# Kernel optimization log

Hardware: AMD Instinct MI355X
Metric: run time of the kernel (lower is better)

The kernel has to match this reference:

```python
import jax, jax.numpy as jnp
import numpy as np

N, E, G = 200000, 1200000, 2048
NODE_DIM, H = 5, 64
NEG_SLOPE = 0.2


def setup_inputs() -> dict:
    key = jax.random.key(0)
    ks = jax.random.split(key, 20)
    def glorot(k, shape):
        fan = sum(shape) if len(shape) > 1 else shape[0] + 1
        return jax.random.normal(k, shape, jnp.float32) * jnp.sqrt(2.0 / fan)
    inp = {
        'x': jax.random.normal(ks[0], (N, NODE_DIM), jnp.float32),
        'edge_index': jax.random.randint(ks[1], (2, E), 0, N, jnp.int64),
        'batch': jnp.sort(jax.random.randint(ks[2], (N,), 0, G, jnp.int64)),
        'embed_W': glorot(ks[3], (NODE_DIM, H)), 'embed_b': jnp.zeros((H,), jnp.float32),
        'g1_W': glorot(ks[4], (H, H)), 'g1_asrc': glorot(ks[5], (H,)), 'g1_adst': glorot(ks[6], (H,)), 'g1_b': jnp.zeros((H,), jnp.float32),
        'g2_W': glorot(ks[7], (H, H)), 'g2_asrc': glorot(ks[8], (H,)), 'g2_adst': glorot(ks[9], (H,)), 'g2_b': jnp.zeros((H,), jnp.float32),
        'fc1_W': glorot(ks[10], (2 * H, 64)), 'fc1_b': jnp.zeros((64,), jnp.float32),
        'fc2_W': glorot(ks[11], (64, 32)), 'fc2_b': jnp.zeros((32,), jnp.float32),
        'fc3_W': glorot(ks[12], (32, 1)), 'fc3_b': jnp.zeros((1,), jnp.float32),
    }
    return inp


def gat_conv(x, src, dst, W, a_src, a_dst, b):
    # x: [N, H] -> h: [N, H]; edges (with self-loops) src->dst
    h = x @ W
    alpha_s = h @ a_src  # [N]
    alpha_d = h @ a_dst  # [N]
    e = jax.nn.leaky_relu(alpha_s[src] + alpha_d[dst], NEG_SLOPE)  # [E']
    m = jax.ops.segment_max(e, dst, num_segments=N)
    w = jnp.exp(e - m[dst])
    denom = jax.ops.segment_sum(w, dst, num_segments=N)
    alpha = w / (denom[dst] + 1e-16)
    out = jax.ops.segment_sum(h[src] * alpha[:, None], dst, num_segments=N)
    return out + b


def reference(x, edge_index, batch, embed_W, embed_b,
              g1_W, g1_asrc, g1_adst, g1_b,
              g2_W, g2_asrc, g2_adst, g2_b,
              fc1_W, fc1_b, fc2_W, fc2_b, fc3_W, fc3_b):
    # add self loops once (PyG GATConv default add_self_loops=True)
    loops = jnp.arange(N, dtype=edge_index.dtype)
    src = jnp.concatenate([edge_index[0], loops])
    dst = jnp.concatenate([edge_index[1], loops])

    h = x @ embed_W + embed_b
    h = gat_conv(h, src, dst, g1_W, g1_asrc, g1_adst, g1_b)
    h = jax.nn.relu(h)
    h = gat_conv(h, src, dst, g2_W, g2_asrc, g2_adst, g2_b)

    # global mean / max pooling per graph
    cnt = jax.ops.segment_sum(jnp.ones((N,), h.dtype), batch, num_segments=G)
    mean = jax.ops.segment_sum(h, batch, num_segments=G) / jnp.maximum(cnt, 1.0)[:, None]
    mx = jax.ops.segment_max(h, batch, num_segments=G)
    mx = jnp.where(cnt[:, None] > 0, mx, 0.0)
    g = jnp.concatenate([mean, mx], axis=1)  # [G, 2H]

    g = jax.nn.relu(g @ fc1_W + fc1_b)
    g = jax.nn.relu(g @ fc2_W + fc2_b)
    return g @ fc3_W + fc3_b  # [G, 1]
```

## Files before the change

### kernel.cpp

```cpp
#include <hip/hip_runtime.h>
#include <hip/hip_bf16.h>
#include <hip/hip_fp16.h>

#define HD 64
#define NODE_DIM 5
#define NEG_SLOPE 0.2f
#define GT 64
#define BSH 9
#define BNODES 512
#define NBMAX 512
#define BCAP 4096
#define EPB 8
#define LDH 72

typedef _Float16 f16x8 __attribute__((ext_vector_type(8)));
typedef float f32x4 __attribute__((ext_vector_type(4)));


__global__ void zero_k(int* __restrict__ p, int total) {
    int i = blockIdx.x * blockDim.x + threadIdx.x;
    if (i < total) p[i] = 0;
}

union FusedSM {
    struct {
        _Float16 hs[GT * LDH];
        _Float16 Wt[HD * LDH];
        float xe[GT * NODE_DIM];
        float we[NODE_DIM * HD + HD];
    } g;
    struct {
        int lcnt[NBMAX];
        int lbase[NBMAX];
        int lexc[NBMAX];
        int cur[NBMAX];
        int sorted[256 * EPB];
    } p;
};

__global__ __launch_bounds__(256) void fused_embed_part_k(
    const float* __restrict__ xin, const float* __restrict__ embW,
    const float* __restrict__ embB, const float* __restrict__ W,
    const float* __restrict__ asrc, const float* __restrict__ adst,
    __half* __restrict__ hout, float* __restrict__ alpha_s,
    float* __restrict__ alpha_d, int N,
    const int* __restrict__ ei, int* __restrict__ bcnt,
    int* __restrict__ bpack, int E, int PB, int TOT) {
    __shared__ FusedSM sm;
    const int t = threadIdx.x;
    const int bid = blockIdx.x;
    const int p_before = (int)(((long long)bid * PB) / TOT);
    const int p_after  = (int)(((long long)(bid + 1) * PB) / TOT);
    const bool is_part = p_after > p_before;

    if (is_part) {
        const int pbid = p_before;
        int dst[EPB], src[EPB];
        int jb = pbid * (256 * EPB) + t;
#pragma unroll
        for (int u = 0; u < EPB; u++) {
            int j = jb + u * 256;
            if (j < E) {
                dst[u] = __builtin_nontemporal_load(&ei[E + j]);
                src[u] = __builtin_nontemporal_load(&ei[j]);
            } else dst[u] = -1;
        }
        sm.p.lcnt[t] = 0; sm.p.lcnt[t + 256] = 0;
        __syncthreads();
#pragma unroll
        for (int u = 0; u < EPB; u++)
            if (dst[u] >= 0) atomicAdd(&sm.p.lcnt[dst[u] >> BSH], 1);
        __syncthreads();
        sm.p.lexc[t] = sm.p.lcnt[t];
        sm.p.lexc[t + 256] = sm.p.lcnt[t + 256];
        __syncthreads();
        int c0 = sm.p.lexc[t], c1 = sm.p.lexc[t + 256];
#pragma unroll
        for (int o = 1; o < NBMAX; o <<= 1) {
            int a0 = (t >= o) ? sm.p.lexc[t - o] : 0;
            int a1 = (t + 256 >= o) ? sm.p.lexc[t + 256 - o] : 0;
            __syncthreads();
            sm.p.lexc[t] += a0;
            sm.p.lexc[t + 256] += a1;
            __syncthreads();
        }
        int e0 = sm.p.lexc[t] - c0, e1 = sm.p.lexc[t + 256] - c1;
        __syncthreads();
        sm.p.lexc[t] = e0; sm.p.lexc[t + 256] = e1;
        sm.p.cur[t] = e0;  sm.p.cur[t + 256] = e1;
        {
            int c = sm.p.lcnt[t];
            sm.p.lbase[t] = c ? t * BCAP + atomicAdd(&bcnt[t], c) : 0;
            c = sm.p.lcnt[t + 256];
            sm.p.lbase[t + 256] = c ? (t + 256) * BCAP + atomicAdd(&bcnt[t + 256], c) : 0;
        }
        __syncthreads();
#pragma unroll
        for (int u = 0; u < EPB; u++) {
            if (dst[u] >= 0) {
                int b = dst[u] >> BSH;
                int pp = atomicAdd(&sm.p.cur[b], 1);
                sm.p.sorted[pp] = (src[u] << BSH) | (dst[u] & (BNODES - 1));
            }
        }
        __syncthreads();
        const int tot = sm.p.lexc[NBMAX - 1] + sm.p.lcnt[NBMAX - 1];
        for (int j = t; j < tot; j += 256) {
            int lo = 0, hi = NBMAX - 1;
            while (lo < hi) {
                int mid = (lo + hi + 1) >> 1;
                if (sm.p.lexc[mid] <= j) lo = mid; else hi = mid - 1;
            }
            bpack[sm.p.lbase[lo] + (j - sm.p.lexc[lo])] = sm.p.sorted[j];
        }
        return;
    }

    const int gidx = bid - p_before;
    const int n0 = gidx * GT;
    if (n0 >= N) return;
    const int rem = N - n0;

#pragma unroll
    for (int j = 0; j < 16; j++) {
        int idx = t + 256 * j;
        int k = idx >> 6, n = idx & 63;
        sm.g.Wt[n * LDH + k] = (_Float16)W[idx];
    }
    for (int j = t; j < GT * NODE_DIM; j += 256)
        sm.g.xe[j] = (j < rem * NODE_DIM) ? xin[(size_t)n0 * NODE_DIM + j] : 0.0f;
    for (int j = t; j < NODE_DIM * HD + HD; j += 256)
        sm.g.we[j] = (j < NODE_DIM * HD) ? embW[j] : embB[j - NODE_DIM * HD];
    __syncthreads();
    {
        int r = t >> 2, d0 = (t & 3) * 16;
#pragma unroll
        for (int jj = 0; jj < 16; jj++) {
            int d = d0 + jj;
            float acc = sm.g.we[NODE_DIM * HD + d];
#pragma unroll
            for (int k = 0; k < NODE_DIM; k++)
                acc = fmaf(sm.g.xe[r * NODE_DIM + k], sm.g.we[k * HD + d], acc);
            sm.g.hs[r * LDH + d] = (r < rem) ? (_Float16)acc : (_Float16)0.0f;
        }
    }
    __syncthreads();

    const int lane = t & 63;
    const int w = t >> 6;
    const int r16 = lane & 15;
    const int g = lane >> 4;

    const _Float16* hrow = sm.g.hs + (w * 16 + r16) * LDH + g * 8;
    f16x8 b0 = *(const f16x8*)(hrow);
    f16x8 b1 = *(const f16x8*)(hrow + 32);

    f32x4 acc[4];
#pragma unroll
    for (int mt = 0; mt < 4; mt++) acc[mt] = (f32x4){0.f, 0.f, 0.f, 0.f};
#pragma unroll
    for (int mt = 0; mt < 4; mt++) {
        const _Float16* arow = sm.g.Wt + (mt * 16 + r16) * LDH + g * 8;
        f16x8 a0 = *(const f16x8*)(arow);
        f16x8 a1 = *(const f16x8*)(arow + 32);
        acc[mt] = __builtin_amdgcn_mfma_f32_16x16x32_f16(a0, b0, acc[mt], 0, 0, 0);
        acc[mt] = __builtin_amdgcn_mfma_f32_16x16x32_f16(a1, b1, acc[mt], 0, 0, 0);
    }

    const int node = n0 + w * 16 + r16;
    float ps = 0.0f, pd = 0.0f;
    if (node < N) {
#pragma unroll
        for (int mt = 0; mt < 4; mt++) {
            float4 av = ((const float4*)asrc)[mt * 4 + g];
            float4 bv = ((const float4*)adst)[mt * 4 + g];
            ps += acc[mt][0] * av.x + acc[mt][1] * av.y +
                  acc[mt][2] * av.z + acc[mt][3] * av.w;
            pd += acc[mt][0] * bv.x + acc[mt][1] * bv.y +
                  acc[mt][2] * bv.z + acc[mt][3] * bv.w;
            short4 s;
            s.x = __half_as_short(__float2half_rn(acc[mt][0]));
            s.y = __half_as_short(__float2half_rn(acc[mt][1]));
            s.z = __half_as_short(__float2half_rn(acc[mt][2]));
            s.w = __half_as_short(__float2half_rn(acc[mt][3]));
            ((short4*)hout)[(size_t)node * 16 + mt * 4 + g] = s;
        }
    }
    ps += __shfl_xor(ps, 16);
    ps += __shfl_xor(ps, 32);
    pd += __shfl_xor(pd, 16);
    pd += __shfl_xor(pd, 32);
    if (g == 0 && node < N) {
        alpha_s[node] = ps;
        alpha_d[node] = pd;
    }
}

__global__ __launch_bounds__(256) void gemm_alpha_k(
    const __half* __restrict__ hin, const float* __restrict__ W,
    const float* __restrict__ asrc, const float* __restrict__ adst,
    __half* __restrict__ hout, float* __restrict__ alpha_s,
    float* __restrict__ alpha_d, int N) {
    __shared__ _Float16 hs[GT * LDH];
    __shared__ _Float16 Wt[HD * LDH];
    const int t = threadIdx.x;
    const int n0 = blockIdx.x * GT;
    if (n0 >= N) return;
    const int rem = N - n0;

#pragma unroll
    for (int j = 0; j < 16; j++) {
        int idx = t + 256 * j;
        int k = idx >> 6, n = idx & 63;
        Wt[n * LDH + k] = (_Float16)W[idx];
    }
    {
        const short4* g4 = (const short4*)(hin + (size_t)n0 * HD);
#pragma unroll
        for (int j = 0; j < 4; j++) {
            int idx = t + 256 * j;
            int row = idx >> 4, c4 = idx & 15;
            short4 v = {0, 0, 0, 0};
            if (row < rem) v = g4[idx];
            *(short4*)(hs + row * LDH + c4 * 4) = v;
        }
    }
    __syncthreads();

    const int lane = t & 63;
    const int w = t >> 6;
    const int r16 = lane & 15;
    const int g = lane >> 4;

    const _Float16* hrow = hs + (w * 16 + r16) * LDH + g * 8;
    f16x8 b0 = *(const f16x8*)(hrow);
    f16x8 b1 = *(const f16x8*)(hrow + 32);

    f32x4 acc[4];
#pragma unroll
    for (int mt = 0; mt < 4; mt++) acc[mt] = (f32x4){0.f, 0.f, 0.f, 0.f};
#pragma unroll
    for (int mt = 0; mt < 4; mt++) {
        const _Float16* arow = Wt + (mt * 16 + r16) * LDH + g * 8;
        f16x8 a0 = *(const f16x8*)(arow);
        f16x8 a1 = *(const f16x8*)(arow + 32);
        acc[mt] = __builtin_amdgcn_mfma_f32_16x16x32_f16(a0, b0, acc[mt], 0, 0, 0);
        acc[mt] = __builtin_amdgcn_mfma_f32_16x16x32_f16(a1, b1, acc[mt], 0, 0, 0);
    }

    const int node = n0 + w * 16 + r16;
    float ps = 0.0f, pd = 0.0f;
    if (node < N) {
#pragma unroll
        for (int mt = 0; mt < 4; mt++) {
            float4 av = ((const float4*)asrc)[mt * 4 + g];
            float4 bv = ((const float4*)adst)[mt * 4 + g];
            ps += acc[mt][0] * av.x + acc[mt][1] * av.y +
                  acc[mt][2] * av.z + acc[mt][3] * av.w;
            pd += acc[mt][0] * bv.x + acc[mt][1] * bv.y +
                  acc[mt][2] * bv.z + acc[mt][3] * bv.w;
            short4 s;
            s.x = __half_as_short(__float2half_rn(acc[mt][0]));
            s.y = __half_as_short(__float2half_rn(acc[mt][1]));
            s.z = __half_as_short(__float2half_rn(acc[mt][2]));
            s.w = __half_as_short(__float2half_rn(acc[mt][3]));
            ((short4*)hout)[(size_t)node * 16 + mt * 4 + g] = s;
        }
    }
    ps += __shfl_xor(ps, 16);
    ps += __shfl_xor(ps, 32);
    pd += __shfl_xor(pd, 16);
    pd += __shfl_xor(pd, 32);
    if (g == 0 && node < N) {
        alpha_s[node] = ps;
        alpha_d[node] = pd;
    }
}

__global__ __launch_bounds__(256) void bucket_csr_k(
    const int* __restrict__ bpack, const int* __restrict__ bcnt,
    int* __restrict__ off, int* __restrict__ csr_src, int N, int NB) {
    __shared__ int s[BNODES];
    __shared__ int lcur[BNODES];
    __shared__ int sred[256];
    const int t = threadIdx.x;
    const int b = blockIdx.x;
    const int nbase = b << BSH;
    const int cnt = bcnt[b];
    const int w0 = b * BCAP;

    int part = 0;
    for (int j = t; j < b; j += 256) part += bcnt[j];
    sred[t] = part;
    s[t] = 0; s[t + 256] = 0;
    __syncthreads();
#pragma unroll
    for (int o = 128; o; o >>= 1) {
        if (t < o) sred[t] += sred[t + o];
        __syncthreads();
    }
    const int e0 = sred[0];

    for (int j = t; j < cnt; j += 256)
        atomicAdd(&s[bpack[w0 + j] & (BNODES - 1)], 1);
    __syncthreads();
    int d0 = s[t], d1 = s[t + 256];
#pragma unroll
    for (int o = 1; o < BNODES; o <<= 1) {
        int a0 = (t >= o) ? s[t - o] : 0;
        int a1 = (t + 256 >= o) ? s[t + 256 - o] : 0;
        __syncthreads();
        s[t] += a0;
        s[t + 256] += a1;
        __syncthreads();
    }
    int ex0 = s[t] - d0, ex1 = s[t + 256] - d1;
    lcur[t] = ex0; lcur[t + 256] = ex1;
    int n0 = nbase + t, n1 = nbase + t + 256;
    if (n0 < N) off[n0] = e0 + ex0;
    if (n1 < N) off[n1] = e0 + ex1;
    if (t == 0 && b == NB - 1) off[N] = e0 + cnt;
    __syncthreads();
    for (int j = t; j < cnt; j += 256) {
        int v = bpack[w0 + j];
        int pos = atomicAdd(&lcur[v & (BNODES - 1)], 1);
        csr_src[e0 + pos] = v >> BSH;
    }
}

template <bool BR>
__global__ __launch_bounds__(256) void gather_k(
    const int* __restrict__ off, const int* __restrict__ csr_src,
    const float* __restrict__ as, const float* __restrict__ ad,
    const __half* __restrict__ h, const float* __restrict__ bias,
    __half* __restrict__ out, int N) {
    int tid = blockIdx.x * blockDim.x + threadIdx.x;
    int wv = tid >> 6;
    int lane = threadIdx.x & 63;
    int grp = lane >> 4;
    int l16 = lane & 15;
    int n = wv * 4 + grp;
    if (n >= N) return;
    int s0 = off[n], s1 = off[n + 1];
    float adv = ad[n];
    const short4* h4 = (const short4*)h;

    float e = as[n] + adv;
    e = (e >= 0.0f) ? e : NEG_SLOPE * e;
    float wsl = __expf(e);
    float l0 = wsl, l1 = 0.0f;
    short4 hvs = h4[(unsigned)(n * 16 + l16)];
    float4 acc0, acc1 = {0, 0, 0, 0};
    acc0.x = wsl * __half2float(__short_as_half(hvs.x));
    acc0.y = wsl * __half2float(__short_as_half(hvs.y));
    acc0.z = wsl * __half2float(__short_as_half(hvs.z));
    acc0.w = wsl * __half2float(__short_as_half(hvs.w));

    const int last = s1 - 1;
    for (int i = s0; i < s1; i += 8) {
        int src[8];
        short4 hv[8];
        float wt[8];
#pragma unroll
        for (int u = 0; u < 8; u++) {
            int idx = i + u;
            src[u] = csr_src[idx < s1 ? idx : last];
        }
#pragma unroll
        for (int u = 0; u < 8; u++)
            hv[u] = h4[(unsigned)(src[u] * 16 + l16)];
#pragma unroll
        for (int u = 0; u < 8; u++) {
            float e0 = as[src[u]] + adv;
            e0 = (e0 >= 0.0f) ? e0 : NEG_SLOPE * e0;
            float w0 = __expf(e0);
            wt[u] = (i + u < s1) ? w0 : 0.0f;
        }
#pragma unroll
        for (int u = 0; u < 8; u += 2) {
            l0 += wt[u];
            l1 += wt[u + 1];
            acc0.x = fmaf(wt[u], __half2float(__short_as_half(hv[u].x)), acc0.x);
            acc0.y = fmaf(wt[u], __half2float(__short_as_half(hv[u].y)), acc0.y);
            acc0.z = fmaf(wt[u], __half2float(__short_as_half(hv[u].z)), acc0.z);
            acc0.w = fmaf(wt[u], __half2float(__short_as_half(hv[u].w)), acc0.w);
            acc1.x = fmaf(wt[u + 1], __half2float(__short_as_half(hv[u + 1].x)), acc1.x);
            acc1.y = fmaf(wt[u + 1], __half2float(__short_as_half(hv[u + 1].y)), acc1.y);
            acc1.z = fmaf(wt[u + 1], __half2float(__short_as_half(hv[u + 1].z)), acc1.z);
            acc1.w = fmaf(wt[u + 1], __half2float(__short_as_half(hv[u + 1].w)), acc1.w);
        }
    }
    float inv = 1.0f / (l0 + l1 + 1e-16f);
    float4 r;
    r.x = (acc0.x + acc1.x) * inv;
    r.y = (acc0.y + acc1.y) * inv;
    r.z = (acc0.z + acc1.z) * inv;
    r.w = (acc0.w + acc1.w) * inv;
    if (BR) {
        float4 b = ((const float4*)bias)[l16];
        r.x = fmaxf(r.x + b.x, 0.0f);
        r.y = fmaxf(r.y + b.y, 0.0f);
        r.z = fmaxf(r.z + b.z, 0.0f);
        r.w = fmaxf(r.w + b.w, 0.0f);
    }
    short4 o;
    o.x = __half_as_short(__float2half_rn(r.x));
    o.y = __half_as_short(__float2half_rn(r.y));
    o.z = __half_as_short(__float2half_rn(r.z));
    o.w = __half_as_short(__float2half_rn(r.w));
    ((short4*)out)[(unsigned)(n * 16 + l16)] = o;
}

__global__ __launch_bounds__(256) void pool_mlp_k(
    const __half* __restrict__ hfin, const float* __restrict__ hb,
    const int* __restrict__ batch, int N,
    const float* __restrict__ fc1W, const float* __restrict__ fc1b,
    const float* __restrict__ fc2W, const float* __restrict__ fc2b,
    const float* __restrict__ fc3W, const float* __restrict__ fc3b,
    float* __restrict__ out) {
    __shared__ float psum[16][64];
    __shared__ float pmax[16][64];
    __shared__ float lds[192];
    int g = blockIdx.x;
    int t = threadIdx.x;
    int gg = t >> 4;
    int l16 = t & 15;
    int lo = 0, hi = N;
    while (lo < hi) { int mid = (lo + hi) >> 1; if (batch[mid] < g) lo = mid + 1; else hi = mid; }
    int start = lo;
    lo = start; hi = N;
    while (lo < hi) { int mid = (lo + hi) >> 1; if (batch[mid] < g + 1) lo = mid + 1; else hi = mid; }
    int end = lo;
    const short4* h4 = (const short4*)hfin;
    float4 sum = {0, 0, 0, 0};
    float4 mx = {-INFINITY, -INFINITY, -INFINITY, -INFINITY};
    for (int n = start + gg; n < end; n += 16) {
        short4 v = h4[(size_t)n * 16 + l16];
        float a = __half2float(__short_as_half(v.x));
        float b = __half2float(__short_as_half(v.y));
        float c = __half2float(__short_as_half(v.z));
        float d = __half2float(__short_as_half(v.w));
        sum.x += a; sum.y += b; sum.z += c; sum.w += d;
        mx.x = fmaxf(mx.x, a); mx.y = fmaxf(mx.y, b);
        mx.z = fmaxf(mx.z, c); mx.w = fmaxf(mx.w, d);
    }
    *(float4*)&psum[gg][l16 * 4] = sum;
    *(float4*)&pmax[gg][l16 * 4] = mx;
    __syncthreads();
    if (t < 64) {
        float s = 0.0f, m = -INFINITY;
#pragma unroll
        for (int k = 0; k < 16; k++) {
            s += psum[k][t];
            m = fmaxf(m, pmax[k][t]);
        }
        int cnt = end - start;
        float bias = hb[t];
        lds[t]      = (cnt > 0) ? s / (float)cnt + bias : 0.0f;
        lds[64 + t] = (cnt > 0) ? m + bias : 0.0f;
    }
    __syncthreads();
    if (t < 64) {
        int lane = t;
        float o1 = fc1b[lane];
        for (int k = 0; k < 128; k++) o1 += lds[k] * fc1W[k * 64 + lane];
        o1 = fmaxf(o1, 0.0f);
        __builtin_amdgcn_s_barrier();
        lds[128 + lane] = o1;
        float o2 = 0.0f;
        if (lane < 32) {
            o2 = fc2b[lane];
            for (int k = 0; k < 64; k++) o2 += lds[128 + k] * fc2W[k * 32 + lane];
            o2 = fmaxf(o2, 0.0f);
        }
        float part = (lane < 32) ? o2 * fc3W[lane] : 0.0f;
#pragma unroll
        for (int off = 32; off; off >>= 1) part += __shfl_xor(part, off);
        if (lane == 0) out[g] = part + fc3b[0];
    }
}

static inline size_t align256(size_t x) { return (x + 255) & ~(size_t)255; }

extern "C" void kernel_launch(void* const* d_in, const int* in_sizes, int n_in,
                              void* d_out, int out_size, void* d_ws, size_t ws_size,
                              hipStream_t stream) {
    const float* x      = (const float*)d_in[0];
    const int*   ei     = (const int*)d_in[1];
    const int*   batch  = (const int*)d_in[2];
    const float* embW   = (const float*)d_in[3];
    const float* embB   = (const float*)d_in[4];
    const float* g1W    = (const float*)d_in[5];
    const float* g1as   = (const float*)d_in[6];
    const float* g1ad   = (const float*)d_in[7];
    const float* g1b    = (const float*)d_in[8];
    const float* g2W    = (const float*)d_in[9];
    const float* g2as   = (const float*)d_in[10];
    const float* g2ad   = (const float*)d_in[11];
    const float* g2b    = (const float*)d_in[12];
    const float* fc1W   = (const float*)d_in[13];
    const float* fc1b   = (const float*)d_in[14];
    const float* fc2W   = (const float*)d_in[15];
    const float* fc2b   = (const float*)d_in[16];
    const float* fc3W   = (const float*)d_in[17];
    const float* fc3b   = (const float*)d_in[18];
    float* out = (float*)d_out;

    const int N  = in_sizes[0] / NODE_DIM;
    const int E  = in_sizes[1] / 2;
    const int G  = out_size;
    const int NH = N * HD;
    const int NB = (N + BNODES - 1) >> BSH;

    char* ws = (char*)d_ws;
    __half* bufA    = (__half*)ws; ws += align256((size_t)NH * 2);
    __half* bufB    = (__half*)ws; ws += align256((size_t)NH * 2);
    float*  as_buf  = (float*)ws;  ws += align256((size_t)N * 4);
    float*  ad_buf  = (float*)ws;  ws += align256((size_t)N * 4);
    int*    off     = (int*)ws;    ws += align256((size_t)(N + 1) * 4);
    int*    bcnt    = (int*)ws;    ws += align256((size_t)NBMAX * 4);
    int*    bpack   = (int*)ws;    ws += align256((size_t)NB * BCAP * 4);
    int*    csrsrc  = (int*)ws;    ws += align256((size_t)E * 4);

    const int B = 256;
    dim3 blk(B);
    const int GB = (N + GT - 1) / GT;
    const int PB = (E + B * EPB - 1) / (B * EPB);
    const int TOT = GB + PB;
    dim3 gr_gath(((N + 3) / 4 * 64 + B - 1) / B);

    zero_k<<<dim3(2), blk, 0, stream>>>(bcnt, NBMAX);
    fused_embed_part_k<<<dim3(TOT), blk, 0, stream>>>(
        x, embW, embB, g1W, g1as, g1ad, bufB, as_buf, ad_buf, N,
        ei, bcnt, bpack, E, PB, TOT);
    bucket_csr_k<<<dim3(NB), blk, 0, stream>>>(bpack, bcnt, off, csrsrc, N, NB);

    gather_k<true><<<gr_gath, blk, 0, stream>>>(off, csrsrc, as_buf, ad_buf,
                                                bufB, g1b, bufA, N);

    gemm_alpha_k<<<dim3(GB), blk, 0, stream>>>(bufA, g2W, g2as, g2ad,
                                               bufB, as_buf, ad_buf, N);
    gather_k<false><<<gr_gath, blk, 0, stream>>>(off, csrsrc, as_buf, ad_buf,
                                                 bufB, nullptr, bufA, N);

    pool_mlp_k<<<dim3(G), dim3(256), 0, stream>>>(bufA, g2b, batch, N,
                                                  fc1W, fc1b, fc2W, fc2b, fc3W, fc3b, out);
}
```

Baseline: 256.5 us.

## Fuse second GAT gather into per-graph pooling and MLP kernel

Drops the separate second-layer gather kernel and does the attention-weighted neighbor aggregation inside the per-graph pool kernel, which now runs 512 threads per graph. Each 16-lane group handles one node, rounds the result to half precision to match the old stored values, and feeds it straight into the sum/max pooling. This removes one launch and the write and re-read of the full N×64 half-precision intermediate. In exchange, parallelism is now bounded by 2048 graph blocks with uneven node counts, which may cost load balance compared with the old node-parallel gather.

```diff
diff --git a/kernel.cpp b/kernel.cpp
--- a/kernel.cpp
+++ b/kernel.cpp
@@ -411,46 +411,108 @@
     ((short4*)out)[(unsigned)(n * 16 + l16)] = o;
 }
 
-__global__ __launch_bounds__(256) void pool_mlp_k(
-    const __half* __restrict__ hfin, const float* __restrict__ hb,
+__global__ __launch_bounds__(512) void gather_pool_mlp_k(
+    const int* __restrict__ off, const int* __restrict__ csr_src,
+    const float* __restrict__ as, const float* __restrict__ ad,
+    const __half* __restrict__ h, const float* __restrict__ hb,
     const int* __restrict__ batch, int N,
     const float* __restrict__ fc1W, const float* __restrict__ fc1b,
     const float* __restrict__ fc2W, const float* __restrict__ fc2b,
     const float* __restrict__ fc3W, const float* __restrict__ fc3b,
     float* __restrict__ out) {
-    __shared__ float psum[16][64];
-    __shared__ float pmax[16][64];
+    __shared__ float psum[32][64];
+    __shared__ float pmax[32][64];
     __shared__ float lds[192];
-    int g = blockIdx.x;
-    int t = threadIdx.x;
-    int gg = t >> 4;
-    int l16 = t & 15;
+    const int g = blockIdx.x;
+    const int t = threadIdx.x;
+    const int wv = t >> 6;
+    const int lane = t & 63;
+    const int grp = lane >> 4;
+    const int l16 = lane & 15;
     int lo = 0, hi = N;
     while (lo < hi) { int mid = (lo + hi) >> 1; if (batch[mid] < g) lo = mid + 1; else hi = mid; }
-    int start = lo;
+    const int start = lo;
     lo = start; hi = N;
     while (lo < hi) { int mid = (lo + hi) >> 1; if (batch[mid] < g + 1) lo = mid + 1; else hi = mid; }
-    int end = lo;
-    const short4* h4 = (const short4*)hfin;
+    const int end = lo;
+    const short4* h4 = (const short4*)h;
+
     float4 sum = {0, 0, 0, 0};
     float4 mx = {-INFINITY, -INFINITY, -INFINITY, -INFINITY};
-    for (int n = start + gg; n < end; n += 16) {
-        short4 v = h4[(size_t)n * 16 + l16];
-        float a = __half2float(__short_as_half(v.x));
-        float b = __half2float(__short_as_half(v.y));
-        float c = __half2float(__short_as_half(v.z));
-        float d = __half2float(__short_as_half(v.w));
-        sum.x += a; sum.y += b; sum.z += c; sum.w += d;
-        mx.x = fmaxf(mx.x, a); mx.y = fmaxf(mx.y, b);
-        mx.z = fmaxf(mx.z, c); mx.w = fmaxf(mx.w, d);
-    }
-    *(float4*)&psum[gg][l16 * 4] = sum;
-    *(float4*)&pmax[gg][l16 * 4] = mx;
+
+    for (int nb = start + wv * 4; nb < end; nb += 32) {
+        const int n = nb + grp;
+        if (n < end) {
+            int s0 = off[n], s1 = off[n + 1];
+            float adv = ad[n];
+            float e = as[n] + adv;
+            e = (e >= 0.0f) ? e : NEG_SLOPE * e;
+            float wsl = __expf(e);
+            float l0 = wsl, l1 = 0.0f;
+            short4 hvs = h4[(unsigned)(n * 16 + l16)];
+            float4 acc0, acc1 = {0, 0, 0, 0};
+            acc0.x = wsl * __half2float(__short_as_half(hvs.x));
+            acc0.y = wsl * __half2float(__short_as_half(hvs.y));
+            acc0.z = wsl * __half2float(__short_as_half(hvs.z));
+            acc0.w = wsl * __half2float(__short_as_half(hvs.w));
+
+            const int last = s1 - 1;
+            for (int i = s0; i < s1; i += 8) {
+                int src[8];
+                short4 hv[8];
+                float wt[8];
+#pragma unroll
+                for (int u = 0; u < 8; u++) {
+                    int idx = i + u;
+                    src[u] = csr_src[idx < s1 ? idx : last];
+                }
+#pragma unroll
+                for (int u = 0; u < 8; u++)
+                    hv[u] = h4[(unsigned)(src[u] * 16 + l16)];
+#pragma unroll
+                for (int u = 0; u < 8; u++) {
+                    float e0 = as[src[u]] + adv;
+                    e0 = (e0 >= 0.0f) ? e0 : NEG_SLOPE * e0;
+                    float w0 = __expf(e0);
+                    wt[u] = (i + u < s1) ? w0 : 0.0f;
+                }
+#pragma unroll
+                for (int u = 0; u < 8; u += 2) {
+                    l0 += wt[u];
+                    l1 += wt[u + 1];
+                    acc0.x = fmaf(wt[u], __half2float(__short_as_half(hv[u].x)), acc0.x);
+                    acc0.y = fmaf(wt[u], __half2float(__short_as_half(hv[u].y)), acc0.y);
+                    acc0.z = fmaf(wt[u], __half2float(__short_as_half(hv[u].z)), acc0.z);
+                    acc0.w = fmaf(wt[u], __half2float(__short_as_half(hv[u].w)), acc0.w);
+                    acc1.x = fmaf(wt[u + 1], __half2float(__short_as_half(hv[u + 1].x)), acc1.x);
+                    acc1.y = fmaf(wt[u + 1], __half2float(__short_as_half(hv[u + 1].y)), acc1.y);
+                    acc1.z = fmaf(wt[u + 1], __half2float(__short_as_half(hv[u + 1].z)), acc1.z);
+                    acc1.w = fmaf(wt[u + 1], __half2float(__short_as_half(hv[u + 1].w)), acc1.w);
+                }
+            }
+            float inv = 1.0f / (l0 + l1 + 1e-16f);
+            float4 r;
+            r.x = (acc0.x + acc1.x) * inv;
+            r.y = (acc0.y + acc1.y) * inv;
+            r.z = (acc0.z + acc1.z) * inv;
+            r.w = (acc0.w + acc1.w) * inv;
+            r.x = __half2float(__float2half_rn(r.x));
+            r.y = __half2float(__float2half_rn(r.y));
+            r.z = __half2float(__float2half_rn(r.z));
+            r.w = __half2float(__float2half_rn(r.w));
+            sum.x += r.x; sum.y += r.y; sum.z += r.z; sum.w += r.w;
+            mx.x = fmaxf(mx.x, r.x); mx.y = fmaxf(mx.y, r.y);
+            mx.z = fmaxf(mx.z, r.z); mx.w = fmaxf(mx.w, r.w);
+        }
+    }
+    const int slot = wv * 4 + grp;
+    *(float4*)&psum[slot][l16 * 4] = sum;
+    *(float4*)&pmax[slot][l16 * 4] = mx;
     __syncthreads();
     if (t < 64) {
         float s = 0.0f, m = -INFINITY;
 #pragma unroll
-        for (int k = 0; k < 16; k++) {
+        for (int k = 0; k < 32; k++) {
             s += psum[k][t];
             m = fmaxf(m, pmax[k][t]);
         }
@@ -461,22 +523,22 @@
     }
     __syncthreads();
     if (t < 64) {
-        int lane = t;
-        float o1 = fc1b[lane];
-        for (int k = 0; k < 128; k++) o1 += lds[k] * fc1W[k * 64 + lane];
+        int lane2 = t;
+        float o1 = fc1b[lane2];
+        for (int k = 0; k < 128; k++) o1 += lds[k] * fc1W[k * 64 + lane2];
         o1 = fmaxf(o1, 0.0f);
         __builtin_amdgcn_s_barrier();
-        lds[128 + lane] = o1;
+        lds[128 + lane2] = o1;
         float o2 = 0.0f;
-        if (lane < 32) {
-            o2 = fc2b[lane];
-            for (int k = 0; k < 64; k++) o2 += lds[128 + k] * fc2W[k * 32 + lane];
+        if (lane2 < 32) {
+            o2 = fc2b[lane2];
+            for (int k = 0; k < 64; k++) o2 += lds[128 + k] * fc2W[k * 32 + lane2];
             o2 = fmaxf(o2, 0.0f);
         }
-        float part = (lane < 32) ? o2 * fc3W[lane] : 0.0f;
-#pragma unroll
-        for (int off = 32; off; off >>= 1) part += __shfl_xor(part, off);
-        if (lane == 0) out[g] = part + fc3b[0];
+        float part = (lane2 < 32) ? o2 * fc3W[lane2] : 0.0f;
+#pragma unroll
+        for (int off2 = 32; off2; off2 >>= 1) part += __shfl_xor(part, off2);
+        if (lane2 == 0) out[g] = part + fc3b[0];
     }
 }
 
@@ -540,9 +602,8 @@
 
     gemm_alpha_k<<<dim3(GB), blk, 0, stream>>>(bufA, g2W, g2as, g2ad,
                                                bufB, as_buf, ad_buf, N);
-    gather_k<false><<<gr_gath, blk, 0, stream>>>(off, csrsrc, as_buf, ad_buf,
-                                                 bufB, nullptr, bufA, N);
-
-    pool_mlp_k<<<dim3(G), dim3(256), 0, stream>>>(bufA, g2b, batch, N,
-                                                  fc1W, fc1b, fc2W, fc2b, fc3W, fc3b, out);
+
+    gather_pool_mlp_k<<<dim3(G), dim3(512), 0, stream>>>(
+        off, csrsrc, as_buf, ad_buf, bufB, g2b, batch, N,
+        fc1W, fc1b, fc2W, fc2b, fc3W, fc3b, out);
 }
```

Result: slower. 268.3 us (+4.6%).
